# Kernel tuning notes

Hardware: AMD Instinct MI355X
Metric: run time of the kernel (lower is better)

Reference implementation:

```python
import jax, jax.numpy as jnp
import numpy as np

D = 1024
H = 16
DH = D // H  # 64
EPS = 1e-6


def setup_inputs() -> dict:
    key = jax.random.key(0)
    ks = jax.random.split(key, 8)
    N, NQ, NK = 8, 1024, 1024
    queries = jax.random.normal(ks[0], (N, NQ, D), dtype=jnp.float32)
    keys = jax.random.normal(ks[1], (N, NK, D), dtype=jnp.float32)
    values = jax.random.normal(ks[2], (N, NK, D), dtype=jnp.float32)
    mask = jax.random.uniform(ks[3], (H * N, NQ, NK), dtype=jnp.float32)
    s = 1.0 / np.sqrt(D)
    Wq = jax.random.normal(ks[4], (H, DH, D), dtype=jnp.float32) * s  # per-head Linear(d, d_head) weights
    Wk = jax.random.normal(ks[5], (H, DH, D), dtype=jnp.float32) * s
    Wv = jax.random.normal(ks[6], (H, DH, D), dtype=jnp.float32) * s
    Wo = jax.random.normal(ks[7], (D, D), dtype=jnp.float32) * s
    return {"queries": queries, "keys": keys, "values": values, "mask": mask,
            "Wq": Wq, "Wk": Wk, "Wv": Wv, "Wo": Wo}


def reference(queries, keys, values, mask, Wq, Wk, Wv, Wo):
    N, NQ, _ = queries.shape
    NK = keys.shape[1]
    # per-head projections, fused into one batched einsum (head-major like torch.cat(dim=0))
    q = jnp.einsum('nqd,hed->hnqe', queries, Wq)  # [H, N, NQ, DH]
    k = jnp.einsum('nkd,hed->hnke', keys, Wk)
    v = jnp.einsum('nkd,hed->hnke', values, Wv)
    scores = jnp.einsum('hnqe,hnke->hnqk', q, k) / jnp.sqrt(jnp.float32(DH))
    att = jax.nn.softmax(scores, axis=-1)  # [H, N, NQ, NK]
    m = mask.reshape(H, N, NQ, NK)
    att = att * m
    att = att / (att.sum(axis=-1, keepdims=True) + EPS)
    o = jnp.einsum('hnqk,hnke->hnqe', att, v)  # [H, N, NQ, DH]
    # concat heads along feature dim: [N, NQ, H*DH]
    o = o.transpose(1, 2, 0, 3).reshape(N, NQ, D)
    return o @ Wo.T
```

## Files before the change

kernel.cpp:

```cpp
#include <hip/hip_runtime.h>
#include <stdint.h>

#define DEV static __device__ __forceinline__

typedef __attribute__((ext_vector_type(8))) short shortx8;
typedef __attribute__((ext_vector_type(4))) float floatx4;
typedef __attribute__((ext_vector_type(4))) unsigned short ushortx4;


DEV unsigned short f2bf(float x) {
  unsigned int u = __float_as_uint(x);
  u += 0x7fffu + ((u >> 16) & 1u);
  return (unsigned short)(u >> 16);
}

DEV void async16(const void* g, void* l) {
  __builtin_amdgcn_global_load_lds(
      (const __attribute__((address_space(1))) void*)g,
      (__attribute__((address_space(3))) void*)l, 16, 0, 0);
}

__global__ __launch_bounds__(256) void cast_w4(const float* __restrict__ w0,
                                               const float* __restrict__ w1,
                                               const float* __restrict__ w2,
                                               const float* __restrict__ w3,
                                               unsigned short* __restrict__ o0,
                                               unsigned short* __restrict__ o1,
                                               unsigned short* __restrict__ o2,
                                               unsigned short* __restrict__ o3) {
  int i = blockIdx.x * 256 + threadIdx.x;
  const float* in; unsigned short* out;
  switch (blockIdx.y) {
    case 0: in = w0; out = o0; break;
    case 1: in = w1; out = o1; break;
    case 2: in = w2; out = o2; break;
    default: in = w3; out = o3; break;
  }
  const floatx4* src = (const floatx4*)in;
  floatx4 a = src[2 * i];
  floatx4 b = src[2 * i + 1];
  shortx8 o;
  o[0] = (short)f2bf(a[0]); o[1] = (short)f2bf(a[1]);
  o[2] = (short)f2bf(a[2]); o[3] = (short)f2bf(a[3]);
  o[4] = (short)f2bf(b[0]); o[5] = (short)f2bf(b[1]);
  o[6] = (short)f2bf(b[2]); o[7] = (short)f2bf(b[3]);
  ((shortx8*)out)[i] = o;
}

__global__ __launch_bounds__(256) void cast_x3(const float* __restrict__ x0,
                                               const float* __restrict__ x1,
                                               const float* __restrict__ x2,
                                               unsigned short* __restrict__ o0,
                                               unsigned short* __restrict__ o1,
                                               unsigned short* __restrict__ o2) {
  int i = blockIdx.x * 256 + threadIdx.x;
  const float* in; unsigned short* out;
  switch (blockIdx.y) {
    case 0: in = x0; out = o0; break;
    case 1: in = x1; out = o1; break;
    default: in = x2; out = o2; break;
  }
  const floatx4* src = (const floatx4*)in;
  floatx4 a = src[2 * i];
  floatx4 b = src[2 * i + 1];
  shortx8 o;
  o[0] = (short)f2bf(a[0]); o[1] = (short)f2bf(a[1]);
  o[2] = (short)f2bf(a[2]); o[3] = (short)f2bf(a[3]);
  o[4] = (short)f2bf(b[0]); o[5] = (short)f2bf(b[1]);
  o[6] = (short)f2bf(b[2]); o[7] = (short)f2bf(b[3]);
  ((shortx8*)out)[i] = o;
}

template <int MODE>
__global__ __launch_bounds__(256) void gemm_bt(const unsigned short* __restrict__ A,
                                               const unsigned short* __restrict__ B,
                                               void* __restrict__ Cout) {
  __shared__ __align__(16) unsigned short As[128 * 32];
  __shared__ __align__(16) unsigned short Bs[128 * 32];
  const int tid  = threadIdx.x;
  const int lane = tid & 63;
  const int wave = tid >> 6;
  const int wm = wave & 1, wn = wave >> 1;
  const int l16 = lane & 15, quad = lane >> 4;
  const int rowBase = blockIdx.y * 128;
  const int colBase = blockIdx.x * 128;

  floatx4 acc[4][4] = {};

  for (int kt = 0; kt < 32; ++kt) {
    __syncthreads();
#pragma unroll
    for (int i = 0; i < 2; ++i) {
      int c = i * 256 + tid;
      int r = c >> 2, kq = c & 3;
      async16(A + (size_t)(rowBase + r) * 1024 + kt * 32 + kq * 8, &As[c * 8]);
      async16(B + (size_t)(colBase + r) * 1024 + kt * 32 + kq * 8, &Bs[c * 8]);
    }
    __syncthreads();
    shortx8 af[4], bfr[4];
#pragma unroll
    for (int t = 0; t < 4; ++t) {
      af[t]  = *(const shortx8*)&As[(wm * 64 + t * 16 + l16) * 32 + quad * 8];
      bfr[t] = *(const shortx8*)&Bs[(wn * 64 + t * 16 + l16) * 32 + quad * 8];
    }
#pragma unroll
    for (int mt = 0; mt < 4; ++mt)
#pragma unroll
      for (int nt = 0; nt < 4; ++nt)
        acc[mt][nt] = __builtin_amdgcn_mfma_f32_16x16x32_bf16(af[mt], bfr[nt], acc[mt][nt], 0, 0, 0);
  }

#pragma unroll
  for (int mt = 0; mt < 4; ++mt) {
#pragma unroll
    for (int nt = 0; nt < 4; ++nt) {
      int col  = colBase + wn * 64 + nt * 16 + l16;
      int row0 = rowBase + wm * 64 + mt * 16 + quad * 4;
      if (MODE == 0) {
        unsigned short* O = (unsigned short*)Cout;
        int h = col >> 6, e = col & 63;
#pragma unroll
        for (int r = 0; r < 4; ++r) {
          int row = row0 + r;
          int n = row >> 10, seq = row & 1023;
          O[(size_t)((h * 8 + n) * 1024 + seq) * 64 + e] = f2bf(acc[mt][nt][r]);
        }
      } else if (MODE == 1) {
        unsigned short* O = (unsigned short*)Cout;
        int h = col >> 6, e = col & 63;
        int n = row0 >> 10, seq0 = row0 & 1023;
        ushortx4 pk;
        pk[0] = f2bf(acc[mt][nt][0]); pk[1] = f2bf(acc[mt][nt][1]);
        pk[2] = f2bf(acc[mt][nt][2]); pk[3] = f2bf(acc[mt][nt][3]);
        *(ushortx4*)&O[(size_t)((h * 8 + n) * 64 + e) * 1024 + seq0] = pk;
      } else {
        float* O = (float*)Cout;
#pragma unroll
        for (int r = 0; r < 4; ++r)
          O[(size_t)(row0 + r) * 1024 + col] = acc[mt][nt][r];
      }
    }
  }
}

__global__ __launch_bounds__(256) void attn_kernel(const unsigned short* __restrict__ Q,
                                                   const unsigned short* __restrict__ K,
                                                   const unsigned short* __restrict__ Vt,
                                                   const float* __restrict__ mask,
                                                   unsigned short* __restrict__ O) {
  __shared__ __align__(16) unsigned short Pl[4 * 32 * 72];
  const int tid = threadIdx.x, lane = tid & 63, wave = tid >> 6;
  const int l16 = lane & 15, quad = lane >> 4;
  const int hn = blockIdx.y;
  const int qt = blockIdx.x;
  const int h = hn >> 3, n = hn & 7;
  const float SC = 0.18033688011112042f;

  const unsigned short* Qb = Q + (size_t)hn * 65536;
  const unsigned short* Kb = K + (size_t)hn * 65536;
  const unsigned short* Vb = Vt + (size_t)hn * 65536;
  const float* Mb = mask + (size_t)hn * 1048576;
  const int q0 = qt * 128 + wave * 32;

  shortx8 qf[2][2];
#pragma unroll
  for (int rt = 0; rt < 2; ++rt)
#pragma unroll
    for (int ks = 0; ks < 2; ++ks)
      qf[rt][ks] = *(const shortx8*)&Qb[(size_t)(q0 + rt * 16 + l16) * 64 + ks * 32 + quad * 8];

  floatx4 oacc[2][4] = {};
  float lsum[2][4] = {};

  unsigned short* Pw = &Pl[wave * 32 * 72];

  for (int kt = 0; kt < 16; ++kt) {
    const int kbase = kt * 64;
    shortx8 kf[4][2];
#pragma unroll
    for (int ct = 0; ct < 4; ++ct)
#pragma unroll
      for (int ks = 0; ks < 2; ++ks)
        kf[ct][ks] = *(const shortx8*)&Kb[(size_t)(kbase + ct * 16 + l16) * 64 + ks * 32 + quad * 8];

#pragma unroll
    for (int rt = 0; rt < 2; ++rt) {
      float mk[4][4];
      const float* Mrow = Mb + (size_t)(q0 + rt * 16 + quad * 4) * 1024 + kbase;
#pragma unroll
      for (int r = 0; r < 4; ++r)
#pragma unroll
        for (int ct = 0; ct < 4; ++ct)
          mk[ct][r] = Mrow[(size_t)r * 1024 + ct * 16 + l16];

      floatx4 s[4] = {};
#pragma unroll
      for (int ct = 0; ct < 4; ++ct)
#pragma unroll
        for (int ks = 0; ks < 2; ++ks)
          s[ct] = __builtin_amdgcn_mfma_f32_16x16x32_bf16(qf[rt][ks], kf[ct][ks], s[ct], 0, 0, 0);

#pragma unroll
      for (int ct = 0; ct < 4; ++ct)
#pragma unroll
        for (int r = 0; r < 4; ++r) {
          float p = exp2f(s[ct][r] * SC);
          float pm = p * mk[ct][r];
          lsum[rt][r] += pm;
          Pw[(rt * 16 + quad * 4 + r) * 72 + ct * 16 + l16] = f2bf(pm);
        }
    }

    shortx8 pf[2][2];
#pragma unroll
    for (int rt = 0; rt < 2; ++rt)
#pragma unroll
      for (int ks = 0; ks < 2; ++ks)
        pf[rt][ks] = *(const shortx8*)&Pw[(rt * 16 + l16) * 72 + ks * 32 + quad * 8];
#pragma unroll
    for (int nt = 0; nt < 4; ++nt) {
      shortx8 vf0 = *(const shortx8*)&Vb[(size_t)(nt * 16 + l16) * 1024 + kbase + quad * 8];
      shortx8 vf1 = *(const shortx8*)&Vb[(size_t)(nt * 16 + l16) * 1024 + kbase + 32 + quad * 8];
#pragma unroll
      for (int rt = 0; rt < 2; ++rt) {
        oacc[rt][nt] = __builtin_amdgcn_mfma_f32_16x16x32_bf16(pf[rt][0], vf0, oacc[rt][nt], 0, 0, 0);
        oacc[rt][nt] = __builtin_amdgcn_mfma_f32_16x16x32_bf16(pf[rt][1], vf1, oacc[rt][nt], 0, 0, 0);
      }
    }
  }

#pragma unroll
  for (int off = 8; off >= 1; off >>= 1)
#pragma unroll
    for (int rt = 0; rt < 2; ++rt)
#pragma unroll
      for (int r = 0; r < 4; ++r)
        lsum[rt][r] += __shfl_xor(lsum[rt][r], off, 64);

  float inv[2][4];
#pragma unroll
  for (int rt = 0; rt < 2; ++rt)
#pragma unroll
    for (int r = 0; r < 4; ++r)
      inv[rt][r] = 1.0f / (lsum[rt][r] + 1e-20f);

#pragma unroll
  for (int rt = 0; rt < 2; ++rt)
#pragma unroll
    for (int nt = 0; nt < 4; ++nt)
#pragma unroll
      for (int r = 0; r < 4; ++r) {
        int qg = q0 + rt * 16 + quad * 4 + r;
        O[(size_t)(n * 1024 + qg) * 1024 + h * 64 + nt * 16 + l16] =
            f2bf(oacc[rt][nt][r] * inv[rt][r]);
      }
}

extern "C" void kernel_launch(void* const* d_in, const int* in_sizes, int n_in,
                              void* d_out, int out_size, void* d_ws, size_t ws_size,
                              hipStream_t stream) {
  const float* queries = (const float*)d_in[0];
  const float* keys    = (const float*)d_in[1];
  const float* values  = (const float*)d_in[2];
  const float* mask    = (const float*)d_in[3];
  const float* Wq      = (const float*)d_in[4];
  const float* Wk      = (const float*)d_in[5];
  const float* Wv      = (const float*)d_in[6];
  const float* Wo      = (const float*)d_in[7];

  char* ws = (char*)d_ws;
  unsigned short* Xq  = (unsigned short*)(ws);
  unsigned short* Xk  = (unsigned short*)(ws + (16u << 20));
  unsigned short* Xv  = (unsigned short*)(ws + (32u << 20));
  unsigned short* Wqb = (unsigned short*)(ws + (48u << 20));
  unsigned short* Wkb = (unsigned short*)(ws + (50u << 20));
  unsigned short* Wvb = (unsigned short*)(ws + (52u << 20));
  unsigned short* Wob = (unsigned short*)(ws + (54u << 20));
  unsigned short* Qp  = (unsigned short*)(ws + (56u << 20));
  unsigned short* Kp  = (unsigned short*)(ws + (72u << 20));
  unsigned short* Vt  = (unsigned short*)(ws + (88u << 20));
  unsigned short* Ob  = Xq;
  float* out = (float*)d_out;

  const int NX8 = 8 * 1024 * 1024 / 8;
  const int NW8 = 16 * 64 * 1024 / 8;
  dim3 blk(256);

  cast_w4<<<dim3(NW8 / 256, 4), blk, 0, stream>>>(Wq, Wk, Wv, Wo, Wqb, Wkb, Wvb, Wob);
  cast_x3<<<dim3(NX8 / 256, 3), blk, 0, stream>>>(queries, keys, values, Xq, Xk, Xv);

  gemm_bt<0><<<dim3(8, 64), blk, 0, stream>>>(Xq, Wqb, (void*)Qp);
  gemm_bt<0><<<dim3(8, 64), blk, 0, stream>>>(Xk, Wkb, (void*)Kp);
  gemm_bt<1><<<dim3(8, 64), blk, 0, stream>>>(Xv, Wvb, (void*)Vt);

  attn_kernel<<<dim3(8, 128), blk, 0, stream>>>(Qp, Kp, Vt, mask, Ob);

  gemm_bt<2><<<dim3(8, 64), blk, 0, stream>>>(Ob, Wob, (void*)out);
}
```

Baseline: 961.1 us.

## Merge cast and QKV GEMM launches, remap attention blocks, add setprio and packed bf16 converts

Combines the two cast kernels into one launch and the three QKV projection GEMMs into a single 3D-grid launch, which cuts launch overhead and raises occupancy per launch. The attention kernel remaps block indices so that consecutive blocks cover different heads and batches, double-buffers the per-wave P scratch in LDS, raises wave priority around the MFMA sections, and uses the hardware packed bf16 conversion instruction. The packed conversion rounds the same way as the software version, so numerics should not change. Several unrelated tweaks are bundled, and some of them may have little effect.

```diff
diff --git a/kernel.cpp b/kernel.cpp
--- a/kernel.cpp
+++ b/kernel.cpp
@@ -6,6 +6,7 @@
 typedef __attribute__((ext_vector_type(8))) short shortx8;
 typedef __attribute__((ext_vector_type(4))) float floatx4;
 typedef __attribute__((ext_vector_type(4))) unsigned short ushortx4;
+typedef __attribute__((ext_vector_type(4))) unsigned int uintx4;
 
 
 DEV unsigned short f2bf(float x) {
@@ -14,67 +15,128 @@
   return (unsigned short)(u >> 16);
 }
 
+DEV unsigned int cvtpk(float lo, float hi) {
+  unsigned int r;
+  asm("v_cvt_pk_bf16_f32 %0, %1, %2" : "=v"(r) : "v"(lo), "v"(hi));
+  return r;
+}
+
 DEV void async16(const void* g, void* l) {
   __builtin_amdgcn_global_load_lds(
       (const __attribute__((address_space(1))) void*)g,
       (__attribute__((address_space(3))) void*)l, 16, 0, 0);
 }
 
-__global__ __launch_bounds__(256) void cast_w4(const float* __restrict__ w0,
-                                               const float* __restrict__ w1,
-                                               const float* __restrict__ w2,
-                                               const float* __restrict__ w3,
-                                               unsigned short* __restrict__ o0,
-                                               unsigned short* __restrict__ o1,
-                                               unsigned short* __restrict__ o2,
-                                               unsigned short* __restrict__ o3) {
-  int i = blockIdx.x * 256 + threadIdx.x;
-  const float* in; unsigned short* out;
-  switch (blockIdx.y) {
-    case 0: in = w0; out = o0; break;
-    case 1: in = w1; out = o1; break;
-    case 2: in = w2; out = o2; break;
-    default: in = w3; out = o3; break;
+__global__ __launch_bounds__(256) void cast_all(
+    const float* __restrict__ xq, const float* __restrict__ xk, const float* __restrict__ xv,
+    const float* __restrict__ wq, const float* __restrict__ wk, const float* __restrict__ wv,
+    const float* __restrict__ wo,
+    unsigned short* __restrict__ oxq, unsigned short* __restrict__ oxk, unsigned short* __restrict__ oxv,
+    unsigned short* __restrict__ owq, unsigned short* __restrict__ owk, unsigned short* __restrict__ owv,
+    unsigned short* __restrict__ owo) {
+  int b = blockIdx.x;
+  const float* in;
+  unsigned short* out;
+  size_t i;
+  if (b < 12288) {
+    int which = b >> 12;
+    in = which == 0 ? xq : (which == 1 ? xk : xv);
+    out = which == 0 ? oxq : (which == 1 ? oxk : oxv);
+    i = (size_t)(b & 4095) * 256 + threadIdx.x;
+  } else {
+    int bb = b - 12288;
+    int which = bb >> 9;
+    in = which == 0 ? wq : (which == 1 ? wk : (which == 2 ? wv : wo));
+    out = which == 0 ? owq : (which == 1 ? owk : (which == 2 ? owv : owo));
+    i = (size_t)(bb & 511) * 256 + threadIdx.x;
   }
   const floatx4* src = (const floatx4*)in;
   floatx4 a = src[2 * i];
-  floatx4 b = src[2 * i + 1];
-  shortx8 o;
-  o[0] = (short)f2bf(a[0]); o[1] = (short)f2bf(a[1]);
-  o[2] = (short)f2bf(a[2]); o[3] = (short)f2bf(a[3]);
-  o[4] = (short)f2bf(b[0]); o[5] = (short)f2bf(b[1]);
-  o[6] = (short)f2bf(b[2]); o[7] = (short)f2bf(b[3]);
-  ((shortx8*)out)[i] = o;
-}
-
-__global__ __launch_bounds__(256) void cast_x3(const float* __restrict__ x0,
-                                               const float* __restrict__ x1,
-                                               const float* __restrict__ x2,
-                                               unsigned short* __restrict__ o0,
-                                               unsigned short* __restrict__ o1,
-                                               unsigned short* __restrict__ o2) {
-  int i = blockIdx.x * 256 + threadIdx.x;
-  const float* in; unsigned short* out;
-  switch (blockIdx.y) {
-    case 0: in = x0; out = o0; break;
-    case 1: in = x1; out = o1; break;
-    default: in = x2; out = o2; break;
-  }
-  const floatx4* src = (const floatx4*)in;
-  floatx4 a = src[2 * i];
-  floatx4 b = src[2 * i + 1];
-  shortx8 o;
-  o[0] = (short)f2bf(a[0]); o[1] = (short)f2bf(a[1]);
-  o[2] = (short)f2bf(a[2]); o[3] = (short)f2bf(a[3]);
-  o[4] = (short)f2bf(b[0]); o[5] = (short)f2bf(b[1]);
-  o[6] = (short)f2bf(b[2]); o[7] = (short)f2bf(b[3]);
-  ((shortx8*)out)[i] = o;
-}
-
-template <int MODE>
-__global__ __launch_bounds__(256) void gemm_bt(const unsigned short* __restrict__ A,
-                                               const unsigned short* __restrict__ B,
-                                               void* __restrict__ Cout) {
+  floatx4 c = src[2 * i + 1];
+  uintx4 o;
+  o[0] = cvtpk(a[0], a[1]);
+  o[1] = cvtpk(a[2], a[3]);
+  o[2] = cvtpk(c[0], c[1]);
+  o[3] = cvtpk(c[2], c[3]);
+  ((uintx4*)out)[i] = o;
+}
+
+
+__global__ __launch_bounds__(256) void gemm_qkv(
+    const unsigned short* __restrict__ Xq, const unsigned short* __restrict__ Xk,
+    const unsigned short* __restrict__ Xv,
+    const unsigned short* __restrict__ Bq, const unsigned short* __restrict__ Bk,
+    const unsigned short* __restrict__ Bv,
+    unsigned short* __restrict__ Oq, unsigned short* __restrict__ Ok,
+    unsigned short* __restrict__ Ov) {
+  __shared__ __align__(16) unsigned short As[128 * 32];
+  __shared__ __align__(16) unsigned short Bs[128 * 32];
+  const int z = blockIdx.z;
+  const unsigned short* A = z == 0 ? Xq : (z == 1 ? Xk : Xv);
+  const unsigned short* B = z == 0 ? Bq : (z == 1 ? Bk : Bv);
+  unsigned short* O = z == 0 ? Oq : (z == 1 ? Ok : Ov);
+
+  const int tid  = threadIdx.x;
+  const int lane = tid & 63;
+  const int wave = tid >> 6;
+  const int wm = wave & 1, wn = wave >> 1;
+  const int l16 = lane & 15, quad = lane >> 4;
+  const int rowBase = blockIdx.y * 128;
+  const int colBase = blockIdx.x * 128;
+
+  floatx4 acc[4][4] = {};
+
+  for (int kt = 0; kt < 32; ++kt) {
+    __syncthreads();
+#pragma unroll
+    for (int i = 0; i < 2; ++i) {
+      int c = i * 256 + tid;
+      int r = c >> 2, kq = c & 3;
+      async16(A + (size_t)(rowBase + r) * 1024 + kt * 32 + kq * 8, &As[c * 8]);
+      async16(B + (size_t)(colBase + r) * 1024 + kt * 32 + kq * 8, &Bs[c * 8]);
+    }
+    __syncthreads();
+    shortx8 af[4], bfr[4];
+#pragma unroll
+    for (int t = 0; t < 4; ++t) {
+      af[t]  = *(const shortx8*)&As[(wm * 64 + t * 16 + l16) * 32 + quad * 8];
+      bfr[t] = *(const shortx8*)&Bs[(wn * 64 + t * 16 + l16) * 32 + quad * 8];
+    }
+#pragma unroll
+    for (int mt = 0; mt < 4; ++mt)
+#pragma unroll
+      for (int nt = 0; nt < 4; ++nt)
+        acc[mt][nt] = __builtin_amdgcn_mfma_f32_16x16x32_bf16(af[mt], bfr[nt], acc[mt][nt], 0, 0, 0);
+  }
+
+#pragma unroll
+  for (int mt = 0; mt < 4; ++mt) {
+#pragma unroll
+    for (int nt = 0; nt < 4; ++nt) {
+      int col  = colBase + wn * 64 + nt * 16 + l16;
+      int row0 = rowBase + wm * 64 + mt * 16 + quad * 4;
+      int h = col >> 6, e = col & 63;
+      if (z != 2) {
+#pragma unroll
+        for (int r = 0; r < 4; ++r) {
+          int row = row0 + r;
+          int n = row >> 10, seq = row & 1023;
+          O[(size_t)((h * 8 + n) * 1024 + seq) * 64 + e] = f2bf(acc[mt][nt][r]);
+        }
+      } else {
+        int n = row0 >> 10, seq0 = row0 & 1023;
+        ushortx4 pk;
+        pk[0] = f2bf(acc[mt][nt][0]); pk[1] = f2bf(acc[mt][nt][1]);
+        pk[2] = f2bf(acc[mt][nt][2]); pk[3] = f2bf(acc[mt][nt][3]);
+        *(ushortx4*)&O[(size_t)((h * 8 + n) * 64 + e) * 1024 + seq0] = pk;
+      }
+    }
+  }
+}
+
+__global__ __launch_bounds__(256) void gemm_out(const unsigned short* __restrict__ A,
+                                                const unsigned short* __restrict__ B,
+                                                float* __restrict__ O) {
   __shared__ __align__(16) unsigned short As[128 * 32];
   __shared__ __align__(16) unsigned short Bs[128 * 32];
   const int tid  = threadIdx.x;
@@ -111,36 +173,15 @@
   }
 
 #pragma unroll
-  for (int mt = 0; mt < 4; ++mt) {
+  for (int mt = 0; mt < 4; ++mt)
 #pragma unroll
     for (int nt = 0; nt < 4; ++nt) {
       int col  = colBase + wn * 64 + nt * 16 + l16;
       int row0 = rowBase + wm * 64 + mt * 16 + quad * 4;
-      if (MODE == 0) {
-        unsigned short* O = (unsigned short*)Cout;
-        int h = col >> 6, e = col & 63;
-#pragma unroll
-        for (int r = 0; r < 4; ++r) {
-          int row = row0 + r;
-          int n = row >> 10, seq = row & 1023;
-          O[(size_t)((h * 8 + n) * 1024 + seq) * 64 + e] = f2bf(acc[mt][nt][r]);
-        }
-      } else if (MODE == 1) {
-        unsigned short* O = (unsigned short*)Cout;
-        int h = col >> 6, e = col & 63;
-        int n = row0 >> 10, seq0 = row0 & 1023;
-        ushortx4 pk;
-        pk[0] = f2bf(acc[mt][nt][0]); pk[1] = f2bf(acc[mt][nt][1]);
-        pk[2] = f2bf(acc[mt][nt][2]); pk[3] = f2bf(acc[mt][nt][3]);
-        *(ushortx4*)&O[(size_t)((h * 8 + n) * 64 + e) * 1024 + seq0] = pk;
-      } else {
-        float* O = (float*)Cout;
-#pragma unroll
-        for (int r = 0; r < 4; ++r)
-          O[(size_t)(row0 + r) * 1024 + col] = acc[mt][nt][r];
-      }
-    }
-  }
+#pragma unroll
+      for (int r = 0; r < 4; ++r)
+        O[(size_t)(row0 + r) * 1024 + col] = acc[mt][nt][r];
+    }
 }
 
 __global__ __launch_bounds__(256) void attn_kernel(const unsigned short* __restrict__ Q,
@@ -148,11 +189,12 @@
                                                    const unsigned short* __restrict__ Vt,
                                                    const float* __restrict__ mask,
                                                    unsigned short* __restrict__ O) {
-  __shared__ __align__(16) unsigned short Pl[4 * 32 * 72];
+  __shared__ __align__(16) unsigned short Pl[2][4 * 32 * 72];
   const int tid = threadIdx.x, lane = tid & 63, wave = tid >> 6;
   const int l16 = lane & 15, quad = lane >> 4;
-  const int hn = blockIdx.y;
-  const int qt = blockIdx.x;
+  const int d = blockIdx.y * 8 + blockIdx.x;
+  const int hn = (d & 7) * 16 + ((d >> 3) & 15);
+  const int qt = d >> 7;
   const int h = hn >> 3, n = hn & 7;
   const float SC = 0.18033688011112042f;
 
@@ -172,10 +214,10 @@
   floatx4 oacc[2][4] = {};
   float lsum[2][4] = {};
 
-  unsigned short* Pw = &Pl[wave * 32 * 72];
-
   for (int kt = 0; kt < 16; ++kt) {
     const int kbase = kt * 64;
+    unsigned short* Pw = &Pl[kt & 1][wave * 32 * 72];
+
     shortx8 kf[4][2];
 #pragma unroll
     for (int ct = 0; ct < 4; ++ct)
@@ -194,21 +236,31 @@
           mk[ct][r] = Mrow[(size_t)r * 1024 + ct * 16 + l16];
 
       floatx4 s[4] = {};
+      __builtin_amdgcn_s_setprio(1);
 #pragma unroll
       for (int ct = 0; ct < 4; ++ct)
 #pragma unroll
         for (int ks = 0; ks < 2; ++ks)
           s[ct] = __builtin_amdgcn_mfma_f32_16x16x32_bf16(qf[rt][ks], kf[ct][ks], s[ct], 0, 0, 0);
-
-#pragma unroll
-      for (int ct = 0; ct < 4; ++ct)
+      __builtin_amdgcn_s_setprio(0);
+
+#pragma unroll
+      for (int ct = 0; ct < 4; ++ct) {
+        float pm[4];
 #pragma unroll
         for (int r = 0; r < 4; ++r) {
           float p = exp2f(s[ct][r] * SC);
-          float pm = p * mk[ct][r];
-          lsum[rt][r] += pm;
-          Pw[(rt * 16 + quad * 4 + r) * 72 + ct * 16 + l16] = f2bf(pm);
+          pm[r] = p * mk[ct][r];
+          lsum[rt][r] += pm[r];
         }
+        unsigned int d01 = cvtpk(pm[0], pm[1]);
+        unsigned int d23 = cvtpk(pm[2], pm[3]);
+        int base = (rt * 16 + quad * 4) * 72 + ct * 16 + l16;
+        Pw[base]       = (unsigned short)d01;
+        Pw[base + 72]  = (unsigned short)(d01 >> 16);
+        Pw[base + 144] = (unsigned short)d23;
+        Pw[base + 216] = (unsigned short)(d23 >> 16);
+      }
     }
 
     shortx8 pf[2][2];
@@ -221,11 +273,13 @@
     for (int nt = 0; nt < 4; ++nt) {
       shortx8 vf0 = *(const shortx8*)&Vb[(size_t)(nt * 16 + l16) * 1024 + kbase + quad * 8];
       shortx8 vf1 = *(const shortx8*)&Vb[(size_t)(nt * 16 + l16) * 1024 + kbase + 32 + quad * 8];
+      __builtin_amdgcn_s_setprio(1);
 #pragma unroll
       for (int rt = 0; rt < 2; ++rt) {
         oacc[rt][nt] = __builtin_amdgcn_mfma_f32_16x16x32_bf16(pf[rt][0], vf0, oacc[rt][nt], 0, 0, 0);
         oacc[rt][nt] = __builtin_amdgcn_mfma_f32_16x16x32_bf16(pf[rt][1], vf1, oacc[rt][nt], 0, 0, 0);
       }
+      __builtin_amdgcn_s_setprio(0);
     }
   }
 
@@ -282,18 +336,11 @@
   unsigned short* Ob  = Xq;
   float* out = (float*)d_out;
 
-  const int NX8 = 8 * 1024 * 1024 / 8;
-  const int NW8 = 16 * 64 * 1024 / 8;
   dim3 blk(256);
 
-  cast_w4<<<dim3(NW8 / 256, 4), blk, 0, stream>>>(Wq, Wk, Wv, Wo, Wqb, Wkb, Wvb, Wob);
-  cast_x3<<<dim3(NX8 / 256, 3), blk, 0, stream>>>(queries, keys, values, Xq, Xk, Xv);
-
-  gemm_bt<0><<<dim3(8, 64), blk, 0, stream>>>(Xq, Wqb, (void*)Qp);
-  gemm_bt<0><<<dim3(8, 64), blk, 0, stream>>>(Xk, Wkb, (void*)Kp);
-  gemm_bt<1><<<dim3(8, 64), blk, 0, stream>>>(Xv, Wvb, (void*)Vt);
-
+  cast_all<<<dim3(14336), blk, 0, stream>>>(queries, keys, values, Wq, Wk, Wv, Wo,
+                                            Xq, Xk, Xv, Wqb, Wkb, Wvb, Wob);
+  gemm_qkv<<<dim3(8, 64, 3), blk, 0, stream>>>(Xq, Xk, Xv, Wqb, Wkb, Wvb, Qp, Kp, Vt);
   attn_kernel<<<dim3(8, 128), blk, 0, stream>>>(Qp, Kp, Vt, mask, Ob);
-
-  gemm_bt<2><<<dim3(8, 64), blk, 0, stream>>>(Ob, Wob, (void*)out);
-}
+  gemm_out<<<dim3(8, 64), blk, 0, stream>>>(Ob, Wob, out);
+}
```

Result: slower. 988.0 us (+2.8%).
